# Optimization experiments

Measured on AMD Instinct MI355X. Metric: run time of the kernel, lower is better.

## Reference

```python
import jax, jax.numpy as jnp
import numpy as np

EMBED_DIM = 1024


def setup_inputs() -> dict:
    key = jax.random.key(0)
    ks = jax.random.split(key, 7)
    B, S, D = 4, 2048, EMBED_DIM
    scale = 1.0 / np.sqrt(D)
    x = jax.random.normal(ks[0], (B, S, D), dtype=jnp.float32)
    # nn.Linear weights stored as [out, in]; we keep [in, out] for x @ W
    Wq = jax.random.normal(ks[1], (D, D), dtype=jnp.float32) * scale
    bq = jax.random.normal(ks[2], (D,), dtype=jnp.float32) * scale
    Wk = jax.random.normal(ks[3], (D, D), dtype=jnp.float32) * scale
    bk = jax.random.normal(ks[4], (D,), dtype=jnp.float32) * scale
    Wv = jax.random.normal(ks[5], (D, D), dtype=jnp.float32) * scale
    bv = jax.random.normal(ks[6], (D,), dtype=jnp.float32) * scale
    return {"x": x, "Wq": Wq, "bq": bq, "Wk": Wk, "bk": bk, "Wv": Wv, "bv": bv}


def reference(x, Wq, bq, Wk, bk, Wv, bv):
    # Single-head attention (num_heads unused in original module).
    q = x @ Wq + bq            # [B, S, D]
    k = x @ Wk + bk            # [B, S, D]
    v = x @ Wv + bv            # [B, S, D]
    inv_sqrt_d = 1.0 / jnp.sqrt(jnp.asarray(x.shape[-1], x.dtype))
    scores = jnp.einsum("bsd,btd->bst", q, k) * inv_sqrt_d  # [B, S, S]
    attn = jax.nn.softmax(scores, axis=-1)
    return jnp.einsum("bst,btd->bsd", attn, v)
```

## Files before the change

kernel.cpp:

```cpp
#include <hip/hip_runtime.h>
#include <hip/hip_bf16.h>


using floatx4 = __attribute__((ext_vector_type(4))) float;
using shortx8 = __attribute__((ext_vector_type(8))) short;
using shortx4 = __attribute__((ext_vector_type(4))) short;

__device__ __forceinline__ short f2bf(float f) {
    __hip_bfloat16 h = __float2bfloat16(f);
    return *reinterpret_cast<short*>(&h);
}
__device__ __forceinline__ float bf2f(short s) {
    unsigned u = (unsigned)(unsigned short)s << 16;
    return __uint_as_float(u);
}

#define MFMA16(a, b, c) __builtin_amdgcn_mfma_f32_16x16x32_bf16((a), (b), (c), 0, 0, 0)

__device__ __forceinline__ void gld_lds16(const void* g, void* l) {
    __builtin_amdgcn_global_load_lds(
        (const __attribute__((address_space(1))) void*)g,
        (__attribute__((address_space(3))) void*)l, 16, 0, 0);
}

__device__ __forceinline__ void gemm_loop(
    const short* __restrict__ A, const short* __restrict__ B,
    size_t lda, size_t ldb, int K,
    short* as_, short* bs_, floatx4 (&acc)[4][4], int w, int l)
{
    const int lr8 = l >> 3;
    const int swz = ((l & 7) ^ lr8) * 8;
    const int lrow = l & 15, quad = l >> 4;
    const int wr = w >> 1, wc = w & 1;
    const int r8r = lrow & 7;
    const short* pa = A + (size_t)(w * 32 + lr8) * lda + swz;
    const short* pb = B + (size_t)(w * 32 + lr8) * ldb + swz;
    short* la = as_ + w * 4 * 512;
    short* lb = bs_ + w * 4 * 512;

    for (int kt = 0; kt < K; kt += 64) {
        for (int c = 0; c < 4; ++c) {
            gld_lds16(pa + (size_t)c * 8 * lda + kt, la + c * 512);
            gld_lds16(pb + (size_t)c * 8 * ldb + kt, lb + c * 512);
        }
        __syncthreads();
        for (int kk = 0; kk < 64; kk += 32) {
            const int xoff = (((kk >> 3) + quad) ^ r8r) << 3;
            shortx8 af[4], bfr[4];
            for (int i = 0; i < 4; ++i)
                af[i] = *reinterpret_cast<const shortx8*>(
                    &as_[(size_t)(wr * 64 + i * 16 + lrow) * 64 + xoff]);
            for (int j = 0; j < 4; ++j)
                bfr[j] = *reinterpret_cast<const shortx8*>(
                    &bs_[(size_t)(wc * 64 + j * 16 + lrow) * 64 + xoff]);
            for (int i = 0; i < 4; ++i)
                for (int j = 0; j < 4; ++j)
                    acc[i][j] = MFMA16(af[i], bfr[j], acc[i][j]);
        }
        __syncthreads();
    }
}

__global__ __launch_bounds__(256) void prep_kernel(
    const float* __restrict__ X,
    const float* __restrict__ Wq, const float* __restrict__ Wk,
    const float* __restrict__ Wv,
    const float* __restrict__ bq, const float* __restrict__ bk,
    const float* __restrict__ bv,
    short* __restrict__ Xb, short* __restrict__ Wt,
    float* __restrict__ bcat, float* __restrict__ sums)
{
    const int id = blockIdx.x, t = threadIdx.x;
    if (id < 4096) {
        size_t i = ((size_t)id * 256 + t) * 8;
        float4 v0 = *reinterpret_cast<const float4*>(X + i);
        float4 v1 = *reinterpret_cast<const float4*>(X + i + 4);
        shortx8 s;
        s[0] = f2bf(v0.x); s[1] = f2bf(v0.y); s[2] = f2bf(v0.z); s[3] = f2bf(v0.w);
        s[4] = f2bf(v1.x); s[5] = f2bf(v1.y); s[6] = f2bf(v1.z); s[7] = f2bf(v1.w);
        *reinterpret_cast<shortx8*>(Xb + i) = s;
    } else if (id < 4864) {
        __shared__ float tl[64][65];
        const int wid = id - 4096;
        const int z = wid >> 8, t16 = wid & 255;
        const float* src = (z == 0) ? Wq : (z == 1) ? Wk : Wv;
        short* dst = Wt + (size_t)z * 1024 * 1024;
        const int k0 = (t16 >> 4) * 64, n0 = (t16 & 15) * 64;
        for (int i = t; i < 64 * 64; i += 256) {
            int r = i >> 6, c = i & 63;
            tl[r][c] = src[(size_t)(k0 + r) * 1024 + n0 + c];
        }
        __syncthreads();
        for (int i = t; i < 64 * 64; i += 256) {
            int r = i >> 6, c = i & 63;
            dst[(size_t)(n0 + r) * 1024 + k0 + c] = f2bf(tl[c][r]);
        }
    } else if (id < 4867) {
        const int z = id - 4864;
        const float* bsrc = (z == 0) ? bq : (z == 1) ? bk : bv;
        for (int i = t; i < 1024; i += 256) bcat[z * 1024 + i] = bsrc[i];
    } else {
        const int sid = id - 4867;
        *reinterpret_cast<float4*>(&sums[sid * 1024 + t * 4]) =
            float4{0.f, 0.f, 0.f, 0.f};
    }
}

__global__ __launch_bounds__(256) void qkv_kernel(
    const short* __restrict__ Xb, const short* __restrict__ Wt,
    const float* __restrict__ bcat, short* __restrict__ dQ,
    short* __restrict__ dK, short* __restrict__ Vt)
{
    __shared__ short as_[128 * 64];
    __shared__ short bs_[128 * 64];
    const int t = threadIdx.x, w = t >> 6, l = t & 63;
    const int m0 = blockIdx.x * 128, n0 = blockIdx.y * 128;
    const int wr = w >> 1, wc = w & 1, lrow = l & 15, quad = l >> 4;
    const int sec = n0 >> 10;

    floatx4 acc[4][4];
    for (int i = 0; i < 4; ++i)
        for (int j = 0; j < 4; ++j) acc[i][j] = floatx4{0.f, 0.f, 0.f, 0.f};

    gemm_loop(Xb + (size_t)m0 * 1024, Wt + (size_t)n0 * 1024,
              1024, 1024, 1024, as_, bs_, acc, w, l);

    short* outN = (sec == 0) ? dQ : dK;
    for (int i = 0; i < 4; ++i) {
        int rbase = m0 + wr * 64 + i * 16 + quad * 4;
        for (int j = 0; j < 4; ++j) {
            int coln = n0 + wc * 64 + j * 16 + lrow;
            int col = coln & 1023;
            float bv = bcat[coln];
            if (sec < 2) {
                for (int r = 0; r < 4; ++r)
                    outN[(size_t)(rbase + r) * 1024 + col] =
                        f2bf(acc[i][j][r] + bv);
            } else {
                int b = rbase >> 11, sl = rbase & 2047;
                shortx4 s;
                for (int r = 0; r < 4; ++r) s[r] = f2bf(acc[i][j][r] + bv);
                *reinterpret_cast<shortx4*>(
                    &Vt[((size_t)b * 1024 + col) * 2048 + sl]) = s;
            }
        }
    }
}

__global__ __launch_bounds__(256) void scores_kernel(
    const short* __restrict__ dQ, const short* __restrict__ dK,
    short* __restrict__ P, float* __restrict__ sums, int row_start)
{
    __shared__ short as_[128 * 64];
    __shared__ short bs_[128 * 64];
    const int t = threadIdx.x, w = t >> 6, l = t & 63;
    const int m0 = blockIdx.x * 128;
    const int n0 = blockIdx.y * 128;
    const int g0 = row_start + m0;
    const int b = g0 >> 11;
    const int wr = w >> 1, wc = w & 1, lrow = l & 15, quad = l >> 4;

    floatx4 acc[4][4];
    for (int i = 0; i < 4; ++i)
        for (int j = 0; j < 4; ++j) acc[i][j] = floatx4{0.f, 0.f, 0.f, 0.f};

    gemm_loop(dQ + (size_t)g0 * 1024, dK + ((size_t)b * 2048 + n0) * 1024,
              1024, 1024, 1024, as_, bs_, acc, w, l);

    for (int i = 0; i < 4; ++i) {
        int rloc = m0 + wr * 64 + i * 16 + quad * 4;
        float rs[4] = {0.f, 0.f, 0.f, 0.f};
        for (int j = 0; j < 4; ++j) {
            int col = n0 + wc * 64 + j * 16 + lrow;
            for (int r = 0; r < 4; ++r) {
                short pb = f2bf(__expf(acc[i][j][r] * 0.03125f - 20.0f));
                P[(size_t)(rloc + r) * 2048 + col] = pb;
                rs[r] += bf2f(pb);
            }
        }
        for (int r = 0; r < 4; ++r)
            for (int m = 1; m <= 8; m <<= 1)
                rs[r] += __shfl_xor(rs[r], m, 64);
        if (lrow == 0)
            for (int r = 0; r < 4; ++r)
                atomicAdd(&sums[row_start + rloc + r], rs[r]);
    }
}

__global__ __launch_bounds__(256) void pv_kernel(
    const short* __restrict__ P, const short* __restrict__ Vt,
    const float* __restrict__ sums, float* __restrict__ Out, int row_start)
{
    __shared__ short as_[128 * 64];
    __shared__ short bs_[128 * 64];
    const int t = threadIdx.x, w = t >> 6, l = t & 63;
    const int m0 = blockIdx.x * 128;
    const int n0 = blockIdx.y * 128;
    const int g0 = row_start + m0;
    const int b = g0 >> 11;
    const int wr = w >> 1, wc = w & 1, lrow = l & 15, quad = l >> 4;

    floatx4 acc[4][4];
    for (int i = 0; i < 4; ++i)
        for (int j = 0; j < 4; ++j) acc[i][j] = floatx4{0.f, 0.f, 0.f, 0.f};

    gemm_loop(P + (size_t)m0 * 2048, Vt + ((size_t)b * 1024 + n0) * 2048,
              2048, 2048, 2048, as_, bs_, acc, w, l);

    for (int i = 0; i < 4; ++i) {
        int rloc = m0 + wr * 64 + i * 16 + quad * 4;
        int rglb = row_start + rloc;
        float is[4];
        for (int r = 0; r < 4; ++r) is[r] = 1.0f / sums[rglb + r];
        for (int j = 0; j < 4; ++j) {
            int col = n0 + wc * 64 + j * 16 + lrow;
            for (int r = 0; r < 4; ++r)
                Out[(size_t)(rglb + r) * 1024 + col] = acc[i][j][r] * is[r];
        }
    }
}

extern "C" void kernel_launch(void* const* d_in, const int* in_sizes, int n_in,
                              void* d_out, int out_size, void* d_ws, size_t ws_size,
                              hipStream_t stream)
{
    const float* x  = (const float*)d_in[0];
    const float* Wq = (const float*)d_in[1];
    const float* bq = (const float*)d_in[2];
    const float* Wk = (const float*)d_in[3];
    const float* bk = (const float*)d_in[4];
    const float* Wv = (const float*)d_in[5];
    const float* bv = (const float*)d_in[6];
    float* out = (float*)d_out;

    short* dQ = (short*)d_out;
    short* dK = dQ + (size_t)8192 * 1024;

    char* ws = (char*)d_ws;
    short* Wt   = (short*)ws;
    float* bcat = (float*)(ws + 6291456);
    float* sums = (float*)(ws + 6291456 + 12288);
    short* Vt   = (short*)(ws + 6291456 + 12288 + 32768);
    char*  region = ws + 6291456 + 12288 + 32768 + 16777216;
    const size_t base = 6291456 + 12288 + 32768 + 16777216;

    size_t avail = ws_size > base ? ws_size - base : 0;
    long rows_fit = (long)(avail / 4096);
    int chunk = (int)(rows_fit & ~127L);
    if (chunk > 8192) chunk = 8192;
    if (chunk < 128) chunk = 128;
    short* Xb = (short*)region;
    short* P  = (short*)region;

    prep_kernel<<<dim3(4875), 256, 0, stream>>>(x, Wq, Wk, Wv, bq, bk, bv,
                                                Xb, Wt, bcat, sums);
    qkv_kernel<<<dim3(64, 24), 256, 0, stream>>>(Xb, Wt, bcat, dQ, dK, Vt);

    for (int rs = 0; rs < 8192; rs += chunk) {
        int rows = 8192 - rs;
        if (rows > chunk) rows = chunk;
        scores_kernel<<<dim3(rows / 128, 16), 256, 0, stream>>>(dQ, dK, P, sums, rs);
        pv_kernel<<<dim3(rows / 128, 8), 256, 0, stream>>>(P, Vt, sums, out, rs);
    }
}
```

Before: 253.3 us.

## Use 256x256 tiles with 8-wave double-buffered pipelined GEMM for QKV and scores

Adds a new GEMM main loop that uses 256x256 output tiles over 512 threads (8 waves), double-buffered LDS and split A/B staging interleaved with MFMA quarters. The loop uses explicit waitcnt, barriers and setprio to overlap global-to-LDS loads with matrix math. The QKV projection and scores kernels switch to it, and the chunk size is rounded to 256 rows. Each loaded tile is reused more, cutting global traffic, but 64 KB LDS and large accumulators per block limit occupancy, and the grid has fewer blocks, which risks tail imbalance on a many-CU device.

```diff
diff --git a/kernel.cpp b/kernel.cpp
--- a/kernel.cpp
+++ b/kernel.cpp
@@ -21,6 +21,150 @@
     __builtin_amdgcn_global_load_lds(
         (const __attribute__((address_space(1))) void*)g,
         (__attribute__((address_space(3))) void*)l, 16, 0, 0);
+}
+
+template<int MH>
+__device__ __forceinline__ void rdA(const short* sAb, int wm, int lrow,
+                                    int xo0, int xo1, shortx8 (&af)[4][2]) {
+    const short* base = sAb + ((wm << 7) + (MH << 6) + lrow) * 64;
+#pragma unroll
+    for (int i = 0; i < 4; ++i) {
+        af[i][0] = *reinterpret_cast<const shortx8*>(base + i * 1024 + xo0);
+        af[i][1] = *reinterpret_cast<const shortx8*>(base + i * 1024 + xo1);
+    }
+}
+template<int NH>
+__device__ __forceinline__ void rdB(const short* sBb, int wn, int lrow,
+                                    int xo0, int xo1, shortx8 (&bf)[4][2]) {
+    const short* base = sBb + ((wn << 6) + (NH << 5) + lrow) * 64;
+#pragma unroll
+    for (int j = 0; j < 2; ++j) {
+        bf[NH * 2 + j][0] = *reinterpret_cast<const shortx8*>(base + j * 1024 + xo0);
+        bf[NH * 2 + j][1] = *reinterpret_cast<const shortx8*>(base + j * 1024 + xo1);
+    }
+}
+template<int MH, int NH>
+__device__ __forceinline__ void mfq(shortx8 (&af)[4][2], shortx8 (&bf)[4][2],
+                                    floatx4 (&acc)[8][4]) {
+    __builtin_amdgcn_s_setprio(1);
+#pragma unroll
+    for (int i = 0; i < 4; ++i) {
+#pragma unroll
+        for (int j = 0; j < 2; ++j) {
+            acc[MH * 4 + i][NH * 2 + j] =
+                MFMA16(af[i][0], bf[NH * 2 + j][0], acc[MH * 4 + i][NH * 2 + j]);
+            acc[MH * 4 + i][NH * 2 + j] =
+                MFMA16(af[i][1], bf[NH * 2 + j][1], acc[MH * 4 + i][NH * 2 + j]);
+        }
+    }
+    __builtin_amdgcn_s_setprio(0);
+}
+
+__device__ __forceinline__ void gemm256_loop8(
+    const short* __restrict__ A, const short* __restrict__ B,
+    int lda, int ldb, int K,
+    short* sA, short* sB, floatx4 (&acc)[8][4], int t)
+{
+    const int w = t >> 6, l = t & 63;
+    const int wm = w >> 2, wn = w & 3;
+    const int lrow = l & 15, quad = l >> 4, r8 = lrow & 7;
+    const int xo0 = (quad ^ r8) << 3;
+    const int xo1 = ((quad + 4) ^ r8) << 3;
+    const int rr = t >> 3;
+    const int gsw = ((t & 7) ^ (rr & 7)) << 3;
+    const short* gA0 = A + (size_t)rr * lda + gsw;
+    const short* gA1 = A + (size_t)(128 + rr) * lda + gsw;
+    const short* gB0 = B + (size_t)rr * ldb + gsw;
+    const short* gB1 = B + (size_t)(128 + rr) * ldb + gsw;
+    const int wofs = w << 9;
+
+    auto stage = [&](const short* g, int ld, int kt, short* ldsb) {
+        const short* p = g + kt;
+        gld_lds16(p, ldsb + wofs);
+        gld_lds16(p + (size_t)(ld << 6), ldsb + wofs + 4096);
+    };
+
+    shortx8 af[4][2], bf[4][2];
+    const int NT = K >> 6;
+
+    stage(gA0, lda, 0, sA);
+    stage(gA1, lda, 0, sA + 8192);
+    stage(gB0, ldb, 0, sB);
+    stage(gB1, ldb, 0, sB + 8192);
+    stage(gB0, ldb, 64, sB + 16384);
+    stage(gB1, ldb, 64, sB + 16384 + 8192);
+    asm volatile("s_waitcnt vmcnt(4)" ::: "memory");
+    __builtin_amdgcn_s_barrier();
+
+    for (int T = 0; T < NT; T += 2) {
+        const bool more = (T + 2) < NT;
+        const int ktA1 = (T + 1) << 6;
+        const int ktN2 = (T + 2) << 6;
+        const int ktB3 = (T + 3) << 6;
+        short* sA0 = sA;           short* sB0 = sB;
+        short* sA1 = sA + 16384;   short* sB1 = sB + 16384;
+
+        rdA<0>(sA0, wm, lrow, xo0, xo1, af);
+        rdB<0>(sB0, wn, lrow, xo0, xo1, bf);
+        stage(gA0, lda, ktA1, sA1);
+        asm volatile("s_waitcnt lgkmcnt(8)" ::: "memory");
+        __builtin_amdgcn_s_barrier();
+        asm volatile("s_waitcnt lgkmcnt(0)" ::: "memory");
+        __builtin_amdgcn_sched_barrier(0);
+        mfq<0, 0>(af, bf, acc);
+        __builtin_amdgcn_s_barrier();
+        rdB<1>(sB0, wn, lrow, xo0, xo1, bf);
+        stage(gA1, lda, ktA1, sA1 + 8192);
+        __builtin_amdgcn_s_barrier();
+        asm volatile("s_waitcnt lgkmcnt(0)" ::: "memory");
+        __builtin_amdgcn_sched_barrier(0);
+        mfq<0, 1>(af, bf, acc);
+        __builtin_amdgcn_s_barrier();
+        rdA<1>(sA0, wm, lrow, xo0, xo1, af);
+        if (more) stage(gB0, ldb, ktN2, sB0);
+        __builtin_amdgcn_s_barrier();
+        asm volatile("s_waitcnt lgkmcnt(0)" ::: "memory");
+        __builtin_amdgcn_sched_barrier(0);
+        mfq<1, 0>(af, bf, acc);
+        __builtin_amdgcn_s_barrier();
+        if (more) stage(gB1, ldb, ktN2, sB0 + 8192);
+        __builtin_amdgcn_s_barrier();
+        __builtin_amdgcn_sched_barrier(0);
+        mfq<1, 1>(af, bf, acc);
+        if (more) { asm volatile("s_waitcnt vmcnt(4)" ::: "memory"); }
+        else      { asm volatile("s_waitcnt vmcnt(0)" ::: "memory"); }
+        __builtin_amdgcn_s_barrier();
+
+        rdA<0>(sA1, wm, lrow, xo0, xo1, af);
+        rdB<0>(sB1, wn, lrow, xo0, xo1, bf);
+        if (more) stage(gA0, lda, ktN2, sA0);
+        asm volatile("s_waitcnt lgkmcnt(8)" ::: "memory");
+        __builtin_amdgcn_s_barrier();
+        asm volatile("s_waitcnt lgkmcnt(0)" ::: "memory");
+        __builtin_amdgcn_sched_barrier(0);
+        mfq<0, 0>(af, bf, acc);
+        __builtin_amdgcn_s_barrier();
+        rdB<1>(sB1, wn, lrow, xo0, xo1, bf);
+        if (more) stage(gA1, lda, ktN2, sA0 + 8192);
+        __builtin_amdgcn_s_barrier();
+        asm volatile("s_waitcnt lgkmcnt(0)" ::: "memory");
+        __builtin_amdgcn_sched_barrier(0);
+        mfq<0, 1>(af, bf, acc);
+        __builtin_amdgcn_s_barrier();
+        rdA<1>(sA1, wm, lrow, xo0, xo1, af);
+        if (more) stage(gB0, ldb, ktB3, sB1);
+        __builtin_amdgcn_s_barrier();
+        asm volatile("s_waitcnt lgkmcnt(0)" ::: "memory");
+        __builtin_amdgcn_sched_barrier(0);
+        mfq<1, 0>(af, bf, acc);
+        __builtin_amdgcn_s_barrier();
+        if (more) stage(gB1, ldb, ktB3, sB1 + 8192);
+        __builtin_amdgcn_s_barrier();
+        __builtin_amdgcn_sched_barrier(0);
+        mfq<1, 1>(af, bf, acc);
+        if (more) { asm volatile("s_waitcnt vmcnt(4)" ::: "memory"); }
+        __builtin_amdgcn_s_barrier();
+    }
 }
 
 __device__ __forceinline__ void gemm_loop(
@@ -106,40 +250,47 @@
     }
 }
 
-__global__ __launch_bounds__(256) void qkv_kernel(
+__global__ __launch_bounds__(512, 2) void qkv_kernel(
     const short* __restrict__ Xb, const short* __restrict__ Wt,
     const float* __restrict__ bcat, short* __restrict__ dQ,
     short* __restrict__ dK, short* __restrict__ Vt)
 {
-    __shared__ short as_[128 * 64];
-    __shared__ short bs_[128 * 64];
-    const int t = threadIdx.x, w = t >> 6, l = t & 63;
-    const int m0 = blockIdx.x * 128, n0 = blockIdx.y * 128;
-    const int wr = w >> 1, wc = w & 1, lrow = l & 15, quad = l >> 4;
+    __shared__ short sA[2 * 16384];
+    __shared__ short sB[2 * 16384];
+    const int t = threadIdx.x;
+    const int m0 = blockIdx.x * 256, n0 = blockIdx.y * 256;
+    const int w = t >> 6, l = t & 63;
+    const int wm = w >> 2, wn = w & 3, lrow = l & 15, quad = l >> 4;
     const int sec = n0 >> 10;
 
-    floatx4 acc[4][4];
-    for (int i = 0; i < 4; ++i)
+    floatx4 acc[8][4];
+#pragma unroll
+    for (int i = 0; i < 8; ++i)
+#pragma unroll
         for (int j = 0; j < 4; ++j) acc[i][j] = floatx4{0.f, 0.f, 0.f, 0.f};
 
-    gemm_loop(Xb + (size_t)m0 * 1024, Wt + (size_t)n0 * 1024,
-              1024, 1024, 1024, as_, bs_, acc, w, l);
+    gemm256_loop8(Xb + (size_t)m0 * 1024, Wt + (size_t)n0 * 1024,
+                  1024, 1024, 1024, sA, sB, acc, t);
 
     short* outN = (sec == 0) ? dQ : dK;
-    for (int i = 0; i < 4; ++i) {
-        int rbase = m0 + wr * 64 + i * 16 + quad * 4;
+#pragma unroll
+    for (int i = 0; i < 8; ++i) {
+        int rbase = m0 + wm * 128 + i * 16 + quad * 4;
+#pragma unroll
         for (int j = 0; j < 4; ++j) {
-            int coln = n0 + wc * 64 + j * 16 + lrow;
+            int coln = n0 + wn * 64 + j * 16 + lrow;
             int col = coln & 1023;
-            float bv = bcat[coln];
+            float bvv = bcat[coln];
             if (sec < 2) {
+#pragma unroll
                 for (int r = 0; r < 4; ++r)
                     outN[(size_t)(rbase + r) * 1024 + col] =
-                        f2bf(acc[i][j][r] + bv);
+                        f2bf(acc[i][j][r] + bvv);
             } else {
                 int b = rbase >> 11, sl = rbase & 2047;
                 shortx4 s;
-                for (int r = 0; r < 4; ++r) s[r] = f2bf(acc[i][j][r] + bv);
+#pragma unroll
+                for (int r = 0; r < 4; ++r) s[r] = f2bf(acc[i][j][r] + bvv);
                 *reinterpret_cast<shortx4*>(
                     &Vt[((size_t)b * 1024 + col) * 2048 + sl]) = s;
             }
@@ -147,41 +298,49 @@
     }
 }
 
-__global__ __launch_bounds__(256) void scores_kernel(
+__global__ __launch_bounds__(512, 2) void scores_kernel(
     const short* __restrict__ dQ, const short* __restrict__ dK,
     short* __restrict__ P, float* __restrict__ sums, int row_start)
 {
-    __shared__ short as_[128 * 64];
-    __shared__ short bs_[128 * 64];
-    const int t = threadIdx.x, w = t >> 6, l = t & 63;
-    const int m0 = blockIdx.x * 128;
-    const int n0 = blockIdx.y * 128;
+    __shared__ short sA[2 * 16384];
+    __shared__ short sB[2 * 16384];
+    const int t = threadIdx.x;
+    const int m0 = blockIdx.x * 256;
+    const int n0 = blockIdx.y * 256;
     const int g0 = row_start + m0;
     const int b = g0 >> 11;
-    const int wr = w >> 1, wc = w & 1, lrow = l & 15, quad = l >> 4;
-
-    floatx4 acc[4][4];
-    for (int i = 0; i < 4; ++i)
+    const int w = t >> 6, l = t & 63;
+    const int wm = w >> 2, wn = w & 3, lrow = l & 15, quad = l >> 4;
+
+    floatx4 acc[8][4];
+#pragma unroll
+    for (int i = 0; i < 8; ++i)
+#pragma unroll
         for (int j = 0; j < 4; ++j) acc[i][j] = floatx4{0.f, 0.f, 0.f, 0.f};
 
-    gemm_loop(dQ + (size_t)g0 * 1024, dK + ((size_t)b * 2048 + n0) * 1024,
-              1024, 1024, 1024, as_, bs_, acc, w, l);
-
-    for (int i = 0; i < 4; ++i) {
-        int rloc = m0 + wr * 64 + i * 16 + quad * 4;
+    gemm256_loop8(dQ + (size_t)g0 * 1024, dK + ((size_t)b * 2048 + n0) * 1024,
+                  1024, 1024, 1024, sA, sB, acc, t);
+
+#pragma unroll
+    for (int i = 0; i < 8; ++i) {
+        int rloc = m0 + wm * 128 + i * 16 + quad * 4;
         float rs[4] = {0.f, 0.f, 0.f, 0.f};
+#pragma unroll
         for (int j = 0; j < 4; ++j) {
-            int col = n0 + wc * 64 + j * 16 + lrow;
+            int col = n0 + wn * 64 + j * 16 + lrow;
+#pragma unroll
             for (int r = 0; r < 4; ++r) {
                 short pb = f2bf(__expf(acc[i][j][r] * 0.03125f - 20.0f));
                 P[(size_t)(rloc + r) * 2048 + col] = pb;
                 rs[r] += bf2f(pb);
             }
         }
+#pragma unroll
         for (int r = 0; r < 4; ++r)
             for (int m = 1; m <= 8; m <<= 1)
                 rs[r] += __shfl_xor(rs[r], m, 64);
         if (lrow == 0)
+#pragma unroll
             for (int r = 0; r < 4; ++r)
                 atomicAdd(&sums[row_start + rloc + r], rs[r]);
     }
@@ -246,20 +405,20 @@
 
     size_t avail = ws_size > base ? ws_size - base : 0;
     long rows_fit = (long)(avail / 4096);
-    int chunk = (int)(rows_fit & ~127L);
+    int chunk = (int)(rows_fit & ~255L);
     if (chunk > 8192) chunk = 8192;
-    if (chunk < 128) chunk = 128;
+    if (chunk < 256) chunk = 256;
     short* Xb = (short*)region;
     short* P  = (short*)region;
 
     prep_kernel<<<dim3(4875), 256, 0, stream>>>(x, Wq, Wk, Wv, bq, bk, bv,
                                                 Xb, Wt, bcat, sums);
-    qkv_kernel<<<dim3(64, 24), 256, 0, stream>>>(Xb, Wt, bcat, dQ, dK, Vt);
+    qkv_kernel<<<dim3(32, 12), 512, 0, stream>>>(Xb, Wt, bcat, dQ, dK, Vt);
 
     for (int rs = 0; rs < 8192; rs += chunk) {
         int rows = 8192 - rs;
         if (rows > chunk) rows = chunk;
-        scores_kernel<<<dim3(rows / 128, 16), 256, 0, stream>>>(dQ, dK, P, sums, rs);
+        scores_kernel<<<dim3(rows / 256, 8), 512, 0, stream>>>(dQ, dK, P, sums, rs);
         pv_kernel<<<dim3(rows / 128, 8), 256, 0, stream>>>(P, Vt, sums, out, rs);
     }
 }
```

Result: no change. 249.6 us (-1.5%).
